# Optimization experiments

Measured on AMD Instinct MI355X. Metric: run time of the kernel, lower is better.

Reference implementation:

```python
import jax, jax.numpy as jnp
import numpy as np

N, IN, OUT, T = 65536, 256, 256, 8


def setup_inputs() -> dict:
    key = jax.random.key(0)
    k1, k2, k3, k4 = jax.random.split(key, 4)
    x = jax.random.normal(k1, (N, IN), dtype=jnp.float32)
    types = jax.random.randint(k2, (N,), 0, T, dtype=jnp.int32)
    # xavier_uniform for W: limit = sqrt(6 / (fan_in + fan_out)) with fan computed
    # on the last two dims (out_size, in_size)
    limit = float(np.sqrt(6.0 / (IN + OUT)))
    W = jax.random.uniform(k3, (T, OUT, IN), dtype=jnp.float32, minval=-limit, maxval=limit)
    # original inits b to zeros; use small random values so the bias path is exercised
    b = 0.01 * jax.random.normal(k4, (T, OUT), dtype=jnp.float32)
    return {"x": x, "types": types, "W": W, "b": b}


def reference(x, types, W, b):
    # out[i] = W[types[i]] @ x[i] + b[types[i]]
    # Grouped-GEMM expressed as a loop over the small fixed set of types,
    # avoiding the huge [N, OUT, IN] gather of W[types].
    num_types = W.shape[0]
    out = b[types]  # [N, OUT]
    for t in range(num_types):
        mask = (types == t)[:, None]  # [N, 1]
        out = out + jnp.where(mask, x @ W[t].T, jnp.float32(0.0))
    return out
```

## Files before the change

### kernel.cpp

```cpp
#include <hip/hip_runtime.h>
#include <stdint.h>


#define NROWS 65536
#define NTYPES 8
#define KDIM 256
#define ODIM 256
#define BM 64
#define MAX_TILES (NROWS / BM + NTYPES - 1)

typedef __attribute__((ext_vector_type(8))) short short8;
typedef __attribute__((ext_vector_type(4))) float f32x4;

__device__ __forceinline__ unsigned short f2bf(float f) {
    unsigned int u = __float_as_uint(f);
    u += 0x7fffu + ((u >> 16) & 1u);
    return (unsigned short)(u >> 16);
}

__global__ void prep_bucket_kernel(const float* __restrict__ W,
                                   unsigned short* __restrict__ Wp,
                                   const int* __restrict__ types,
                                   int* __restrict__ cnt,
                                   int* __restrict__ idx) {
    const int b = blockIdx.x;
    if (b < 256) {
        const int gid = b * 256 + threadIdx.x;
        const int R   = gid >> 5;
        const int c32 = gid & 31;
        const int t  = R >> 8;
        const int r  = R & 255;
        const int f  = r & 15;
        const int rr = r >> 4;
        const int q  = c32 >> 2;
        const int l  = (c32 & 3) * 16 + rr;
        const float* src = W + (size_t)R * KDIM + c32 * 8;
        const float4 v0 = *(const float4*)src;
        const float4 v1 = *(const float4*)(src + 4);
        ushort4 p0, p1;
        p0.x = f2bf(v0.x); p0.y = f2bf(v0.y); p0.z = f2bf(v0.z); p0.w = f2bf(v0.w);
        p1.x = f2bf(v1.x); p1.y = f2bf(v1.y); p1.z = f2bf(v1.z); p1.w = f2bf(v1.w);
        ushort4* dst = (ushort4*)(Wp + (size_t)(((t * 16 + f) * 8 + q) * 512 + l * 8));
        dst[0] = p0; dst[1] = p1;
    } else {
        __shared__ int h[NTYPES];
        __shared__ int base[NTYPES];
        int i = (b - 256) * 256 + threadIdx.x;
        if (threadIdx.x < NTYPES) h[threadIdx.x] = 0;
        __syncthreads();
        int t = types[i];
        int r = atomicAdd(&h[t], 1);
        __syncthreads();
        if (threadIdx.x < NTYPES)
            base[threadIdx.x] = atomicAdd(&cnt[threadIdx.x], h[threadIdx.x]);
        __syncthreads();
        idx[t * NROWS + base[t] + r] = i;
    }
}

__global__ __launch_bounds__(256, 4)
void gemm_kernel(const float* __restrict__ x,
                 const float* __restrict__ bias,
                 const unsigned short* __restrict__ Wp,
                 const int* __restrict__ cnt,
                 const int* __restrict__ idx,
                 float* __restrict__ out) {
    const int bid = blockIdx.x;
    int t = -1, m0 = 0, count = 0, accum = 0;
    #pragma unroll
    for (int i = 0; i < NTYPES; ++i) {
        int c = cnt[i];
        int ntile = (c + BM - 1) / BM;
        if (t < 0 && bid < accum + ntile) { t = i; m0 = (bid - accum) * BM; count = c; }
        accum += ntile;
    }
    if (t < 0) return;

    __shared__ unsigned short As[BM * KDIM];
    __shared__ int idx_s[BM];
    char* AsB = (char*)As;

    const int tid = threadIdx.x;
    const int wave = tid >> 6;
    const int lane = tid & 63;
    const int lr = lane & 15;
    const int lq = lane >> 4;

    const float4 bv = *(const float4*)(bias + t * ODIM + lr * 16 + wave * 4);

    const int srow = tid >> 4;
    const int sc   = tid & 15;

    #pragma unroll
    for (int p = 0; p < 4; ++p) {
        const int row = p * 16 + srow;
        const int gr = m0 + row;
        const int xr = idx[t * NROWS + (gr < count ? gr : count - 1)];
        if (sc == 0) idx_s[row] = xr;
        const float* xs = x + (size_t)xr * KDIM;
        #pragma unroll
        for (int s = 0; s < 4; ++s) {
            const int slot = s * 16 + sc;
            const float4 v = *(const float4*)(xs + slot * 4);
            ushort4 pk;
            pk.x = f2bf(v.x); pk.y = f2bf(v.y); pk.z = f2bf(v.z); pk.w = f2bf(v.w);
            const int c = slot >> 1;
            *(ushort4*)(AsB + row * 512 + (c ^ (row & 7)) * 16 + (slot & 1) * 8) = pk;
        }
    }
    __syncthreads();

    const unsigned short* Wpt = Wp + (size_t)t * 16 * 8 * 512;

    f32x4 acc[4][4] = {};

    #pragma unroll
    for (int q = 0; q < 8; ++q) {
        short8 bf[4], af[4];
        #pragma unroll
        for (int j = 0; j < 4; ++j)
            bf[j] = *(const short8*)(Wpt + ((size_t)((wave * 4 + j) * 8 + q)) * 512
                                         + lane * 8);
        #pragma unroll
        for (int i = 0; i < 4; ++i) {
            const int row = i * 16 + lr;
            af[i] = *(const short8*)(AsB + row * 512
                                         + (((q << 2) + lq) ^ (row & 7)) * 16);
        }
        #pragma unroll
        for (int i = 0; i < 4; ++i)
            #pragma unroll
            for (int j = 0; j < 4; ++j)
                acc[i][j] = __builtin_amdgcn_mfma_f32_16x16x32_bf16(
                    af[i], bf[j], acc[i][j], 0, 0, 0);
    }

    #pragma unroll
    for (int i = 0; i < 4; ++i) {
        #pragma unroll
        for (int r = 0; r < 4; ++r) {
            const int lm = i * 16 + lq * 4 + r;
            const int gr = m0 + lm;
            if (gr < count) {
                const size_t orow = (size_t)idx_s[lm] * ODIM;
                float4 v;
                v.x = acc[i][0][r] + bv.x;
                v.y = acc[i][1][r] + bv.y;
                v.z = acc[i][2][r] + bv.z;
                v.w = acc[i][3][r] + bv.w;
                *(float4*)(out + orow + lr * 16 + wave * 4) = v;
            }
        }
    }
}

extern "C" void kernel_launch(void* const* d_in, const int* in_sizes, int n_in,
                              void* d_out, int out_size, void* d_ws, size_t ws_size,
                              hipStream_t stream) {
    const float* x     = (const float*)d_in[0];
    const int*   types = (const int*)d_in[1];
    const float* W     = (const float*)d_in[2];
    const float* b     = (const float*)d_in[3];
    float* out = (float*)d_out;

    char* ws = (char*)d_ws;
    int* cnt = (int*)ws;
    int* idx = (int*)(ws + 1024);
    unsigned short* Wp = (unsigned short*)(ws + 1024 + (size_t)NTYPES * NROWS * sizeof(int));

    hipMemsetAsync(cnt, 0, NTYPES * sizeof(int), stream);
    prep_bucket_kernel<<<512, 256, 0, stream>>>(W, Wp, types, cnt, idx);
    gemm_kernel<<<MAX_TILES, 256, 0, stream>>>(x, b, Wp, cnt, idx, out);
}
```

Measured before the change: 146.1 us.

## Pre-gather x into type-bucketed bf16 buffer and load tiles via global_load_lds

Splits bucketing into a histogram pass plus a new gather kernel that converts x rows to bf16 and scatters them into a contiguous, swizzled, per-type padded buffer. The GEMM kernel then streams each 64-row tile straight into LDS with global_load_lds instead of doing indexed fp32 loads and conversion itself. The weight packing layout and the bias/output indexing change to match. This adds an extra kernel launch and an extra round trip of x through memory in bf16, in exchange for contiguous, asynchronous tile loads in the GEMM.

```diff
diff --git a/kernel.cpp b/kernel.cpp
--- a/kernel.cpp
+++ b/kernel.cpp
@@ -18,11 +18,10 @@
     return (unsigned short)(u >> 16);
 }
 
-__global__ void prep_bucket_kernel(const float* __restrict__ W,
-                                   unsigned short* __restrict__ Wp,
-                                   const int* __restrict__ types,
-                                   int* __restrict__ cnt,
-                                   int* __restrict__ idx) {
+__global__ void prep_hist_kernel(const float* __restrict__ W,
+                                 unsigned short* __restrict__ Wp,
+                                 const int* __restrict__ types,
+                                 int* __restrict__ cnt) {
     const int b = blockIdx.x;
     if (b < 256) {
         const int gid = b * 256 + threadIdx.x;
@@ -30,8 +29,8 @@
         const int c32 = gid & 31;
         const int t  = R >> 8;
         const int r  = R & 255;
-        const int f  = r & 15;
-        const int rr = r >> 4;
+        const int f  = r >> 4;
+        const int rr = r & 15;
         const int q  = c32 >> 2;
         const int l  = (c32 & 3) * 16 + rr;
         const float* src = W + (size_t)R * KDIM + c32 * 8;
@@ -44,35 +43,88 @@
         dst[0] = p0; dst[1] = p1;
     } else {
         __shared__ int h[NTYPES];
-        __shared__ int base[NTYPES];
-        int i = (b - 256) * 256 + threadIdx.x;
+        const int i = (b - 256) * 256 + threadIdx.x;
         if (threadIdx.x < NTYPES) h[threadIdx.x] = 0;
         __syncthreads();
-        int t = types[i];
-        int r = atomicAdd(&h[t], 1);
+        atomicAdd(&h[types[i]], 1);
         __syncthreads();
-        if (threadIdx.x < NTYPES)
-            base[threadIdx.x] = atomicAdd(&cnt[threadIdx.x], h[threadIdx.x]);
-        __syncthreads();
-        idx[t * NROWS + base[t] + r] = i;
+        if (threadIdx.x < NTYPES) atomicAdd(&cnt[threadIdx.x], h[threadIdx.x]);
+    }
+}
+
+__global__ __launch_bounds__(256)
+void bucket_gather_kernel(const float* __restrict__ x,
+                          const int* __restrict__ types,
+                          int* __restrict__ cnt,
+                          int* __restrict__ idx,
+                          char* __restrict__ xgB) {
+    __shared__ int h[NTYPES];
+    __shared__ int b2[NTYPES];
+    __shared__ int ps[NTYPES];
+    __shared__ int dst_s[64];
+
+    const int tid = threadIdx.x;
+    const int i0 = blockIdx.x * 64;
+
+    if (tid < NTYPES) h[tid] = 0;
+    __syncthreads();
+
+    int myt = 0, myr = 0;
+    if (tid < 64) {
+        myt = types[i0 + tid];
+        myr = atomicAdd(&h[myt], 1);
+    }
+    __syncthreads();
+    if (tid < NTYPES) b2[tid] = atomicAdd(&cnt[NTYPES + tid], h[tid]);
+    if (tid == 0) {
+        int acc = 0;
+        #pragma unroll
+        for (int t = 0; t < NTYPES; ++t) {
+            ps[t] = acc;
+            acc += ((cnt[t] + 63) >> 6) << 6;
+        }
+    }
+    __syncthreads();
+    if (tid < 64) {
+        const int g = ps[myt] + b2[myt] + myr;
+        dst_s[tid] = g;
+        idx[g] = i0 + tid;
+    }
+    __syncthreads();
+
+    const int wave = tid >> 6;
+    const int lane = tid & 63;
+    const int c = lane >> 1;
+    const int bo = (lane & 1) * 8;
+    #pragma unroll 4
+    for (int k = 0; k < 16; ++k) {
+        const int rr = wave * 16 + k;
+        const int g = dst_s[rr];
+        const float4 v = *(const float4*)(x + (size_t)(i0 + rr) * KDIM + lane * 4);
+        ushort4 p;
+        p.x = f2bf(v.x); p.y = f2bf(v.y); p.z = f2bf(v.z); p.w = f2bf(v.w);
+        *(ushort4*)(xgB + (size_t)g * 512 + ((c ^ (g & 7)) * 16) + bo) = p;
     }
 }
 
 __global__ __launch_bounds__(256, 4)
-void gemm_kernel(const float* __restrict__ x,
-                 const float* __restrict__ bias,
+void gemm_kernel(const float* __restrict__ bias,
                  const unsigned short* __restrict__ Wp,
                  const int* __restrict__ cnt,
                  const int* __restrict__ idx,
+                 const char* __restrict__ xgB,
                  float* __restrict__ out) {
     const int bid = blockIdx.x;
-    int t = -1, m0 = 0, count = 0, accum = 0;
+    int t = -1, m0 = 0, count = 0, accum = 0, rowacc = 0, gbase = 0;
     #pragma unroll
     for (int i = 0; i < NTYPES; ++i) {
-        int c = cnt[i];
-        int ntile = (c + BM - 1) / BM;
-        if (t < 0 && bid < accum + ntile) { t = i; m0 = (bid - accum) * BM; count = c; }
+        const int c = cnt[i];
+        const int ntile = (c + BM - 1) / BM;
+        if (t < 0 && bid < accum + ntile) {
+            t = i; m0 = (bid - accum) * BM; count = c; gbase = rowacc + m0;
+        }
         accum += ntile;
+        rowacc += ntile * BM;
     }
     if (t < 0) return;
 
@@ -86,28 +138,27 @@
     const int lr = lane & 15;
     const int lq = lane >> 4;
 
-    const float4 bv = *(const float4*)(bias + t * ODIM + lr * 16 + wave * 4);
-
-    const int srow = tid >> 4;
-    const int sc   = tid & 15;
-
-    #pragma unroll
-    for (int p = 0; p < 4; ++p) {
-        const int row = p * 16 + srow;
-        const int gr = m0 + row;
-        const int xr = idx[t * NROWS + (gr < count ? gr : count - 1)];
-        if (sc == 0) idx_s[row] = xr;
-        const float* xs = x + (size_t)xr * KDIM;
-        #pragma unroll
-        for (int s = 0; s < 4; ++s) {
-            const int slot = s * 16 + sc;
-            const float4 v = *(const float4*)(xs + slot * 4);
-            ushort4 pk;
-            pk.x = f2bf(v.x); pk.y = f2bf(v.y); pk.z = f2bf(v.z); pk.w = f2bf(v.w);
-            const int c = slot >> 1;
-            *(ushort4*)(AsB + row * 512 + (c ^ (row & 7)) * 16 + (slot & 1) * 8) = pk;
-        }
-    }
+    const int rowlim = count - m0;
+    if (tid < BM)
+        idx_s[tid] = idx[gbase + (tid < rowlim ? tid : rowlim - 1)];
+
+    #pragma unroll
+    for (int it = 0; it < 8; ++it) {
+        const int dbyte = wave * 8192 + it * 1024;
+        const int R0 = wave * 16 + it * 2;
+        const char* src = xgB + (size_t)(gbase + R0 + (lane >> 5)) * 512
+                              + (size_t)(lane & 31) * 16;
+        __builtin_amdgcn_global_load_lds(
+            (const __attribute__((address_space(1))) void*)src,
+            (__attribute__((address_space(3))) void*)(AsB + dbyte),
+            16, 0, 0);
+    }
+
+    float bv[4];
+    #pragma unroll
+    for (int j = 0; j < 4; ++j)
+        bv[j] = bias[t * ODIM + wave * 64 + j * 16 + lr];
+
     __syncthreads();
 
     const unsigned short* Wpt = Wp + (size_t)t * 16 * 8 * 512;
@@ -140,15 +191,11 @@
         #pragma unroll
         for (int r = 0; r < 4; ++r) {
             const int lm = i * 16 + lq * 4 + r;
-            const int gr = m0 + lm;
-            if (gr < count) {
+            if (lm < rowlim) {
                 const size_t orow = (size_t)idx_s[lm] * ODIM;
-                float4 v;
-                v.x = acc[i][0][r] + bv.x;
-                v.y = acc[i][1][r] + bv.y;
-                v.z = acc[i][2][r] + bv.z;
-                v.w = acc[i][3][r] + bv.w;
-                *(float4*)(out + orow + lr * 16 + wave * 4) = v;
+                #pragma unroll
+                for (int j = 0; j < 4; ++j)
+                    out[orow + wave * 64 + j * 16 + lr] = acc[i][j][r] + bv[j];
             }
         }
     }
@@ -165,10 +212,12 @@
 
     char* ws = (char*)d_ws;
     int* cnt = (int*)ws;
-    int* idx = (int*)(ws + 1024);
-    unsigned short* Wp = (unsigned short*)(ws + 1024 + (size_t)NTYPES * NROWS * sizeof(int));
-
-    hipMemsetAsync(cnt, 0, NTYPES * sizeof(int), stream);
-    prep_bucket_kernel<<<512, 256, 0, stream>>>(W, Wp, types, cnt, idx);
-    gemm_kernel<<<MAX_TILES, 256, 0, stream>>>(x, b, Wp, cnt, idx, out);
-}
+    int* idx = (int*)(ws + 4096);
+    unsigned short* Wp = (unsigned short*)(ws + 274432);
+    char* xgB = ws + 1572864;
+
+    hipMemsetAsync(cnt, 0, 64, stream);
+    prep_hist_kernel<<<512, 256, 0, stream>>>(W, Wp, types, cnt);
+    bucket_gather_kernel<<<NROWS / 64, 256, 0, stream>>>(x, types, cnt, idx, xgB);
+    gemm_kernel<<<MAX_TILES, 256, 0, stream>>>(b, Wp, cnt, idx, xgB, out);
+}
```

New measurement: 162.0 us. 10.9% more time.
